# Performance work log

Hardware: AMD Instinct MI355X
Metric: run time of the kernel (lower is better)

Reference implementation:

```python
import jax, jax.numpy as jnp
import numpy as np

N, E, C, H, L, G, K, NC = 50000, 500000, 256, 128, 4, 64, 8, 2
EPS_MSG = 1e-7  # GENConv message eps
EPS_BN = 1e-5   # BatchNorm eps


def setup_inputs() -> dict:
    key = jax.random.key(0)
    ks = jax.random.split(key, 32)
    def nrm(k, shape, scale):
        return jax.random.normal(k, shape, dtype=jnp.float32) * scale
    sC = 1.0 / np.sqrt(C).astype(np.float32)
    sH = 1.0 / np.sqrt(H).astype(np.float32)
    s2H = 1.0 / np.sqrt(2 * H).astype(np.float32)
    return dict(
        x=nrm(ks[0], (N, C), 1.0),
        edge_index=jax.random.randint(ks[1], (2, E), 0, N, dtype=jnp.int32),
        edge_attr=jax.random.uniform(ks[2], (E, 1), dtype=jnp.float32),
        batch=jnp.sort(jax.random.randint(ks[3], (N,), 0, G, dtype=jnp.int32)),
        clinical=nrm(ks[4], (G, K), 1.0),
        lin_src_w=nrm(ks[5], (C, H), sC), lin_src_b=nrm(ks[6], (H,), 0.01),
        lin_dst_w=nrm(ks[7], (C, H), sC), lin_dst_b=nrm(ks[8], (H,), 0.01),
        edge_w=nrm(ks[9], (L, 1, H), 1.0), edge_b=nrm(ks[10], (L, H), 0.01),
        t=0.1 + 0.01 * jax.random.normal(ks[11], (L,), dtype=jnp.float32),
        mlp_w1=nrm(ks[12], (L, H, 2 * H), sH), mlp_b1=nrm(ks[13], (L, 2 * H), 0.01),
        mlp_bn_g=1.0 + nrm(ks[14], (L, 2 * H), 0.1), mlp_bn_b=nrm(ks[15], (L, 2 * H), 0.1),
        mlp_bn_m=nrm(ks[16], (L, 2 * H), 0.1),
        mlp_bn_v=1.0 + jax.random.uniform(ks[17], (L, 2 * H), dtype=jnp.float32),
        mlp_w2=nrm(ks[18], (L, 2 * H, H), s2H), mlp_b2=nrm(ks[19], (L, H), 0.01),
        norm_g=1.0 + nrm(ks[20], (L, H), 0.1), norm_b=nrm(ks[21], (L, H), 0.1),
        norm_m=nrm(ks[22], (L, H), 0.1),
        norm_v=1.0 + jax.random.uniform(ks[23], (L, H), dtype=jnp.float32),
        cls_w=nrm(ks[24], (H + K, NC), 1.0 / np.sqrt(H + K).astype(np.float32)),
        cls_b=nrm(ks[25], (NC,), 0.01),
    )


def _bn(h, g, b, m, v):
    # eval-mode BatchNorm with running stats
    return g * (h - m) * jax.lax.rsqrt(v + EPS_BN) + b


def reference(x, edge_index, edge_attr, batch, clinical,
              lin_src_w, lin_src_b, lin_dst_w, lin_dst_b,
              edge_w, edge_b, t,
              mlp_w1, mlp_b1, mlp_bn_g, mlp_bn_b, mlp_bn_m, mlp_bn_v,
              mlp_w2, mlp_b2, norm_g, norm_b, norm_m, norm_v,
              cls_w, cls_b):
    n = x.shape[0]
    g_count = clinical.shape[0]
    src, dst = edge_index[0], edge_index[1]
    n_layers = t.shape[0]

    def genconv(xs, xd, l):
        # xs: source features feeding messages [N,H]; xd: dst skip features [N,H]
        e = edge_attr @ edge_w[l] + edge_b[l]               # [E,H]
        msg = jax.nn.relu(xs[src] + e) + EPS_MSG            # [E,H]
        z = msg * t[l]
        zmax = jax.ops.segment_max(z, dst, num_segments=n)  # [N,H]
        zmax = jnp.where(jnp.isfinite(zmax), zmax, 0.0)
        ez = jnp.exp(z - zmax[dst])
        denom = jax.ops.segment_sum(ez, dst, num_segments=n)
        agg = jax.ops.segment_sum(msg * ez, dst, num_segments=n) / jnp.maximum(denom, 1e-16)
        out = agg + xd
        # internal MLP [H, 2H, H]: Linear -> BN -> ReLU -> Linear
        hmid = jax.nn.relu(_bn(out @ mlp_w1[l] + mlp_b1[l],
                               mlp_bn_g[l], mlp_bn_b[l], mlp_bn_m[l], mlp_bn_v[l]))
        return hmid @ mlp_w2[l] + mlp_b2[l]

    # layer 0: conv only (per DeepGCN.forward); lin_src / lin_dst project C -> H
    xs0 = x @ lin_src_w + lin_src_b
    xd0 = x @ lin_dst_w + lin_dst_b
    h = genconv(xs0, xd0, 0)

    # layers 1..L-1: res+ block (norm -> act -> conv, residual add); dropout = identity (eval)
    for l in range(1, n_layers):
        r = jax.nn.relu(_bn(h, norm_g[l], norm_b[l], norm_m[l], norm_v[l]))
        h = h + genconv(r, r, l)

    # final norm/act from layer 0
    h = jax.nn.relu(_bn(h, norm_g[0], norm_b[0], norm_m[0], norm_v[0]))

    # global mean pool over graphs
    cnt = jax.ops.segment_sum(jnp.ones((n,), h.dtype), batch, num_segments=g_count)
    pooled = jax.ops.segment_sum(h, batch, num_segments=g_count) / jnp.maximum(cnt, 1.0)[:, None]

    z = jnp.concatenate([pooled, clinical], axis=1)
    return z @ cls_w + cls_b  # [G, num_classes]; squeeze is a no-op for G>1, NC=2
```

## Files before the change

### kernel.cpp

```cpp
#include <hip/hip_runtime.h>
#include <math.h>

#define Nn 50000
#define MPAD 50048
#define Ee 500000
#define Cc 256
#define Hh 128
#define Ll 4
#define Gg 64
#define Kk 8
#define NCc 2

#define NB 196

typedef __attribute__((ext_vector_type(8))) short short8;
typedef __attribute__((ext_vector_type(4))) float f32x4;
typedef __attribute__((ext_vector_type(2))) float f32x2;

#define RFL __builtin_amdgcn_readfirstlane

__device__ __forceinline__ unsigned short f2bf(float f) {
    union { float f; unsigned int u; } v;
    v.f = f;
    unsigned int u = v.u;
    return (unsigned short)((u + 0x7FFFu + ((u >> 16) & 1u)) >> 16);
}
__device__ __forceinline__ float bf2f(unsigned short s) {
    union { float f; unsigned int u; } v;
    v.u = ((unsigned int)s) << 16;
    return v.f;
}
__device__ __forceinline__ float bf2f_lo(unsigned int u) {
    union { float f; unsigned int u; } v;
    v.u = u << 16;
    return v.f;
}
__device__ __forceinline__ float bf2f_hi(unsigned int u) {
    union { float f; unsigned int u; } v;
    v.u = u & 0xffff0000u;
    return v.f;
}


__global__ void hist_kernel(const int* __restrict__ dst, int* __restrict__ deg) {
    int e = blockIdx.x * 256 + threadIdx.x;
    if (e < Ee) atomicAdd(&deg[dst[e]], 1);
}

__global__ __launch_bounds__(256) void bsum_kernel(const int* __restrict__ deg,
                                                   int* __restrict__ bsum) {
    __shared__ int ws[4];
    int t = threadIdx.x;
    int i = blockIdx.x * 256 + t;
    int v = (i < Nn) ? deg[i] : 0;
#pragma unroll
    for (int o = 32; o; o >>= 1) v += __shfl_down(v, o, 64);
    if ((t & 63) == 0) ws[t >> 6] = v;
    __syncthreads();
    if (t == 0) bsum[blockIdx.x] = ws[0] + ws[1] + ws[2] + ws[3];
}

__global__ __launch_bounds__(256) void bscan_kernel(const int* __restrict__ bsum,
                                                    int* __restrict__ boff,
                                                    int* __restrict__ off) {
    __shared__ int sc[256];
    int t = threadIdx.x;
    int v = (t < NB) ? bsum[t] : 0;
    sc[t] = v;
    __syncthreads();
    for (int o = 1; o < 256; o <<= 1) {
        int u = (t >= o) ? sc[t - o] : 0;
        __syncthreads();
        sc[t] += u;
        __syncthreads();
    }
    if (t < NB) boff[t] = sc[t] - v;
    if (t == NB - 1) off[Nn] = sc[t];
}

__global__ __launch_bounds__(256) void offsets_kernel(const int* __restrict__ deg,
                                                      const int* __restrict__ boff,
                                                      int* __restrict__ off,
                                                      int* __restrict__ pos) {
    __shared__ int sc[256];
    int t = threadIdx.x;
    int i = blockIdx.x * 256 + t;
    int v = (i < Nn) ? deg[i] : 0;
    sc[t] = v;
    __syncthreads();
    for (int o = 1; o < 256; o <<= 1) {
        int u = (t >= o) ? sc[t - o] : 0;
        __syncthreads();
        sc[t] += u;
        __syncthreads();
    }
    int excl = sc[t] - v + boff[blockIdx.x];
    if (i < Nn) {
        off[i] = excl;
        pos[i] = excl;
    }
}

__global__ void scatter_kernel(const int* __restrict__ src, const int* __restrict__ dst,
                               const float* __restrict__ attr, int* __restrict__ pos,
                               int2* __restrict__ sedge) {
    int e = blockIdx.x * 256 + threadIdx.x;
    if (e < Ee) {
        int d = dst[e];
        int p = atomicAdd(&pos[d], 1);
        sedge[p] = make_int2(src[e], __float_as_int(attr[e]));
    }
}


__global__ void wconv_kernel(const float* __restrict__ lin_src_w,
                             const float* __restrict__ lin_dst_w,
                             const float* __restrict__ mlp_w1,
                             const float* __restrict__ mlp_w2,
                             unsigned short* __restrict__ wt) {
    int idx = blockIdx.x * 256 + threadIdx.x;
    if (idx >= 327680) return;
    float val;
    if (idx < 65536) {
        int n = idx >> 8, k = idx & 255;
        val = (n < 128) ? lin_src_w[k * 128 + n] : lin_dst_w[k * 128 + (n - 128)];
    } else if (idx < 196608) {
        int r = idx - 65536;
        int l = r >> 15, e = r & 32767;
        int n = e >> 7, k = e & 127;
        val = mlp_w1[(size_t)l * 32768 + k * 256 + n];
    } else {
        int r = idx - 196608;
        int l = r >> 15, e = r & 32767;
        int n = e >> 8, k = e & 255;
        val = mlp_w2[(size_t)l * 32768 + k * 128 + n];
    }
    wt[idx] = f2bf(val);
}


__global__ __launch_bounds__(256) void xconv_kernel(const float* __restrict__ x,
                                                    unsigned short* __restrict__ xbf) {
    int idx = blockIdx.x * 256 + threadIdx.x;
    if (idx >= (Nn * Cc) / 8) return;
    const float4* p = (const float4*)(x) + (size_t)idx * 2;
    float4 v0 = p[0], v1 = p[1];
    unsigned short t[8];
    t[0] = f2bf(v0.x); t[1] = f2bf(v0.y); t[2] = f2bf(v0.z); t[3] = f2bf(v0.w);
    t[4] = f2bf(v1.x); t[5] = f2bf(v1.y); t[6] = f2bf(v1.z); t[7] = f2bf(v1.w);
    *(short8*)(xbf + (size_t)idx * 8) = *(short8*)t;
}

#define GLOAD16(gp, lp)                                                                       \
    __builtin_amdgcn_global_load_lds(                                                         \
        (const __attribute__((address_space(1))) unsigned int*)(gp),                          \
        (__attribute__((address_space(3))) unsigned int*)(lp), 16, 0, 0)


__global__ __launch_bounds__(256) void proj_kernel(
    const unsigned short* __restrict__ A, const unsigned short* __restrict__ Bt,
    const float* __restrict__ bias, const float* __restrict__ bias2,
    unsigned short* __restrict__ Cout) {
    __shared__ __align__(16) unsigned short SH[24576];
    int tid = threadIdx.x;
    int wave = tid >> 6, lane = tid & 63;
    int wr = wave >> 1, wc = wave & 1;
    int lrow = lane & 15, quad = lane >> 4;
    int m0 = blockIdx.y * 128, n0 = blockIdx.x * 128;
    const int K = 256;

    const unsigned short* ag0 = A + (size_t)(m0 + (tid >> 2)) * K + (tid & 3) * 8;
    const unsigned short* ag1 = A + (size_t)(m0 + 64 + (tid >> 2)) * K + (tid & 3) * 8;
    const unsigned short* bg0 = Bt + (size_t)(n0 + (tid >> 2)) * K + (tid & 3) * 8;
    const unsigned short* bg1 = Bt + (size_t)(n0 + 64 + (tid >> 2)) * K + (tid & 3) * 8;

    f32x4 acc[4][4];
#pragma unroll
    for (int i = 0; i < 4; i++)
#pragma unroll
        for (int j = 0; j < 4; j++) acc[i][j] = (f32x4){0.f, 0.f, 0.f, 0.f};

    auto stage = [&](int buf, int koff) {
        GLOAD16(ag0 + koff, SH + buf * 4096 + wave * 512);
        GLOAD16(ag1 + koff, SH + buf * 4096 + 2048 + wave * 512);
        GLOAD16(bg0 + koff, SH + 12288 + buf * 4096 + wave * 512);
        GLOAD16(bg1 + koff, SH + 12288 + buf * 4096 + 2048 + wave * 512);
    };

    const int ntiles = 8;
    stage(0, 0);
    stage(1, 32);
    for (int t = 0; t < ntiles; ++t) {
        if (t + 1 < ntiles) {
            asm volatile("s_waitcnt vmcnt(4)\n\ts_barrier" ::: "memory");
        } else {
            asm volatile("s_waitcnt vmcnt(0)\n\ts_barrier" ::: "memory");
        }
        if (t + 2 < ntiles) stage((t + 2) % 3, (t + 2) * 32);
        int cur = t % 3;
        const unsigned short* As = SH + cur * 4096;
        const unsigned short* Bs = SH + 12288 + cur * 4096;
        short8 af[4], bfr[4];
#pragma unroll
        for (int mt = 0; mt < 4; mt++)
            af[mt] = *(const short8*)&As[(wr * 64 + mt * 16 + lrow) * 32 + quad * 8];
#pragma unroll
        for (int nf = 0; nf < 4; nf++)
            bfr[nf] = *(const short8*)&Bs[(wc * 64 + nf * 16 + lrow) * 32 + quad * 8];
#pragma unroll
        for (int mt = 0; mt < 4; mt++)
#pragma unroll
            for (int nf = 0; nf < 4; nf++)
                acc[mt][nf] = __builtin_amdgcn_mfma_f32_16x16x32_bf16(af[mt], bfr[nf],
                                                                     acc[mt][nf], 0, 0, 0);
    }

    __syncthreads();
    unsigned short* Cl = SH;
#pragma unroll
    for (int nf = 0; nf < 4; nf++) {
        int gc = n0 + wc * 64 + nf * 16 + lrow;
        float bs = (gc >= 128) ? bias2[gc - 128] : bias[gc];
        int col = wc * 64 + nf * 16 + lrow;
#pragma unroll
        for (int mt = 0; mt < 4; mt++)
#pragma unroll
            for (int r = 0; r < 4; r++)
                Cl[(wr * 64 + mt * 16 + quad * 4 + r) * 128 + col] = f2bf(acc[mt][nf][r] + bs);
    }
    __syncthreads();
#pragma unroll
    for (int p = 0; p < 8; p++) {
        int vid = p * 256 + tid;
        int row = vid >> 4, cg = (vid & 15) * 8;
        short8 v = *(const short8*)&Cl[row * 128 + cg];
        *(short8*)(Cout + (size_t)(m0 + row) * 256 + n0 + cg) = v;
    }
}


__global__ __launch_bounds__(256) void mlp_kernel(
    const unsigned short* __restrict__ A,
    const unsigned short* __restrict__ W1,
    const unsigned short* __restrict__ W2,
    const float* __restrict__ b1, const float* __restrict__ bn_g,
    const float* __restrict__ bn_b, const float* __restrict__ bn_m,
    const float* __restrict__ bn_v, const float* __restrict__ b2,
    const float* __restrict__ pn_g, const float* __restrict__ pn_b,
    const float* __restrict__ pn_m, const float* __restrict__ pn_v,
    float* __restrict__ hbuf, unsigned short* __restrict__ rbuf, int rmw) {
    __shared__ __align__(16) unsigned short LDS_[23040];
    unsigned short* Ap = LDS_;
    unsigned short* B1 = LDS_ + 8192;
    unsigned short* Hm = LDS_;
    unsigned short* B2 = LDS_ + 16896;

    int tid = threadIdx.x;
    int wave = tid >> 6, lane = tid & 63;
    int lrow = lane & 15, quad = lane >> 4;
    int m0 = blockIdx.x * 64;

    {
        const unsigned short* as = A + (size_t)(m0 + (tid >> 2)) * 128 + (tid & 3) * 8;
#pragma unroll
        for (int t = 0; t < 4; t++) GLOAD16(as + t * 32, Ap + t * 2048 + wave * 512);
    }
    const unsigned short* w1base = W1 + (size_t)(tid >> 2) * 128 + (tid & 3) * 8;
    auto stageB1 = [&](int s, int b) {
        int h = s >> 2, t = s & 3;
        const unsigned short* p = w1base + (size_t)h * 128 * 128 + t * 32;
        GLOAD16(p, B1 + b * 4096 + wave * 512);
        GLOAD16(p + (size_t)64 * 128, B1 + b * 4096 + 2048 + wave * 512);
    };
    stageB1(0, 0);
    stageB1(1, 1);

    f32x4 acc1a[4][2], acc1b[4][2];
#pragma unroll
    for (int i = 0; i < 4; i++)
#pragma unroll
        for (int j = 0; j < 2; j++) {
            acc1a[i][j] = (f32x4){0.f, 0.f, 0.f, 0.f};
            acc1b[i][j] = (f32x4){0.f, 0.f, 0.f, 0.f};
        }

#pragma unroll
    for (int t = 0; t < 4; t++) {
        asm volatile("s_waitcnt vmcnt(2)\n\ts_barrier" ::: "memory");
        stageB1(t + 2, (t + 2) % 3);
        const unsigned short* Apan = Ap + t * 2048;
        const unsigned short* Bs = B1 + (t % 3) * 4096;
        short8 af[4], bfr[2];
#pragma unroll
        for (int mt = 0; mt < 4; mt++)
            af[mt] = *(const short8*)&Apan[(mt * 16 + lrow) * 32 + quad * 8];
#pragma unroll
        for (int nf = 0; nf < 2; nf++)
            bfr[nf] = *(const short8*)&Bs[(wave * 32 + nf * 16 + lrow) * 32 + quad * 8];
#pragma unroll
        for (int mt = 0; mt < 4; mt++)
#pragma unroll
            for (int nf = 0; nf < 2; nf++)
                acc1a[mt][nf] = __builtin_amdgcn_mfma_f32_16x16x32_bf16(af[mt], bfr[nf],
                                                                       acc1a[mt][nf], 0, 0, 0);
    }
#pragma unroll
    for (int t = 0; t < 4; t++) {
        if (t < 3) {
            asm volatile("s_waitcnt vmcnt(2)\n\ts_barrier" ::: "memory");
        } else {
            asm volatile("s_waitcnt vmcnt(0)\n\ts_barrier" ::: "memory");
        }
        if (t < 2) stageB1(6 + t, (6 + t) % 3);
        const unsigned short* Apan = Ap + t * 2048;
        const unsigned short* Bs = B1 + ((4 + t) % 3) * 4096;
        short8 af[4], bfr[2];
#pragma unroll
        for (int mt = 0; mt < 4; mt++)
            af[mt] = *(const short8*)&Apan[(mt * 16 + lrow) * 32 + quad * 8];
#pragma unroll
        for (int nf = 0; nf < 2; nf++)
            bfr[nf] = *(const short8*)&Bs[(wave * 32 + nf * 16 + lrow) * 32 + quad * 8];
#pragma unroll
        for (int mt = 0; mt < 4; mt++)
#pragma unroll
            for (int nf = 0; nf < 2; nf++)
                acc1b[mt][nf] = __builtin_amdgcn_mfma_f32_16x16x32_bf16(af[mt], bfr[nf],
                                                                       acc1b[mt][nf], 0, 0, 0);
    }
    __syncthreads();

    const unsigned short* w2base = W2 + (size_t)(tid >> 2) * 256 + (tid & 3) * 8;
    auto stageB2 = [&](int s, int b) {
        int h = s >> 3, t = s & 7;
        GLOAD16(w2base + (size_t)h * 64 * 256 + t * 32, B2 + b * 2048 + wave * 512);
    };
    stageB2(0, 0);
    stageB2(1, 1);

#pragma unroll
    for (int nf = 0; nf < 2; nf++) {
        int gc = wave * 32 + nf * 16 + lrow;
        float bs = b1[gc];
        float g = bn_g[gc], bb = bn_b[gc], mm = bn_m[gc];
        float inv = rsqrtf(bn_v[gc] + 1e-5f);
#pragma unroll
        for (int mt = 0; mt < 4; mt++)
#pragma unroll
            for (int r = 0; r < 4; r++) {
                float v = acc1a[mt][nf][r] + bs;
                v = fmaxf(g * (v - mm) * inv + bb, 0.f);
                Hm[(mt * 16 + quad * 4 + r) * 264 + gc] = f2bf(v);
            }
    }
#pragma unroll
    for (int nf = 0; nf < 2; nf++) {
        int gc = 128 + wave * 32 + nf * 16 + lrow;
        float bs = b1[gc];
        float g = bn_g[gc], bb = bn_b[gc], mm = bn_m[gc];
        float inv = rsqrtf(bn_v[gc] + 1e-5f);
#pragma unroll
        for (int mt = 0; mt < 4; mt++)
#pragma unroll
            for (int r = 0; r < 4; r++) {
                float v = acc1b[mt][nf][r] + bs;
                v = fmaxf(g * (v - mm) * inv + bb, 0.f);
                Hm[(mt * 16 + quad * 4 + r) * 264 + gc] = f2bf(v);
            }
    }
    __syncthreads();

    f32x4 acc2a[4], acc2b[4];
#pragma unroll
    for (int i = 0; i < 4; i++) {
        acc2a[i] = (f32x4){0.f, 0.f, 0.f, 0.f};
        acc2b[i] = (f32x4){0.f, 0.f, 0.f, 0.f};
    }
#pragma unroll
    for (int t = 0; t < 8; t++) {
        asm volatile("s_waitcnt vmcnt(1)\n\ts_barrier" ::: "memory");
        stageB2(t + 2, (t + 2) % 3);
        const unsigned short* Bs = B2 + (t % 3) * 2048;
        short8 af[4];
#pragma unroll
        for (int mt = 0; mt < 4; mt++)
            af[mt] = *(const short8*)&Hm[(mt * 16 + lrow) * 264 + t * 32 + quad * 8];
        short8 bf = *(const short8*)&Bs[(wave * 16 + lrow) * 32 + quad * 8];
#pragma unroll
        for (int mt = 0; mt < 4; mt++)
            acc2a[mt] = __builtin_amdgcn_mfma_f32_16x16x32_bf16(af[mt], bf, acc2a[mt], 0, 0, 0);
    }
#pragma unroll
    for (int t = 0; t < 8; t++) {
        if (t < 7) {
            asm volatile("s_waitcnt vmcnt(1)\n\ts_barrier" ::: "memory");
        } else {
            asm volatile("s_waitcnt vmcnt(0)\n\ts_barrier" ::: "memory");
        }
        if (t < 6) stageB2(10 + t, (10 + t) % 3);
        const unsigned short* Bs = B2 + ((8 + t) % 3) * 2048;
        short8 af[4];
#pragma unroll
        for (int mt = 0; mt < 4; mt++)
            af[mt] = *(const short8*)&Hm[(mt * 16 + lrow) * 264 + t * 32 + quad * 8];
        short8 bf = *(const short8*)&Bs[(wave * 16 + lrow) * 32 + quad * 8];
#pragma unroll
        for (int mt = 0; mt < 4; mt++)
            acc2b[mt] = __builtin_amdgcn_mfma_f32_16x16x32_bf16(af[mt], bf, acc2b[mt], 0, 0, 0);
    }
    __syncthreads();

    float* C2 = (float*)LDS_;
    {
        int gc0 = wave * 16 + lrow, gc1 = 64 + wave * 16 + lrow;
        float bs0 = b2[gc0], bs1 = b2[gc1];
#pragma unroll
        for (int mt = 0; mt < 4; mt++)
#pragma unroll
            for (int r = 0; r < 4; r++) {
                C2[(mt * 16 + quad * 4 + r) * 132 + gc0] = acc2a[mt][r] + bs0;
                C2[(mt * 16 + quad * 4 + r) * 132 + gc1] = acc2b[mt][r] + bs1;
            }
    }
    __syncthreads();
#pragma unroll
    for (int p = 0; p < 8; p++) {
        int vid = p * 256 + tid;
        int row = vid >> 5, c4 = (vid & 31) * 4;
        f32x4 v = *(const f32x4*)&C2[row * 132 + c4];
        float* hp = hbuf + (size_t)(m0 + row) * 128 + c4;
        if (rmw) v += *(const f32x4*)hp;
        *(f32x4*)hp = v;
        if (pn_g) {
            f32x4 pg = *(const f32x4*)&pn_g[c4];
            f32x4 pb = *(const f32x4*)&pn_b[c4];
            f32x4 pm = *(const f32x4*)&pn_m[c4];
            f32x4 pv = *(const f32x4*)&pn_v[c4];
            float r0 = fmaxf(pg[0] * (v[0] - pm[0]) * rsqrtf(pv[0] + 1e-5f) + pb[0], 0.f);
            float r1 = fmaxf(pg[1] * (v[1] - pm[1]) * rsqrtf(pv[1] + 1e-5f) + pb[1], 0.f);
            float r2 = fmaxf(pg[2] * (v[2] - pm[2]) * rsqrtf(pv[2] + 1e-5f) + pb[2], 0.f);
            float r3 = fmaxf(pg[3] * (v[3] - pm[3]) * rsqrtf(pv[3] + 1e-5f) + pb[3], 0.f);
            unsigned int w0 = (unsigned int)f2bf(r0) | ((unsigned int)f2bf(r1) << 16);
            unsigned int w1 = (unsigned int)f2bf(r2) | ((unsigned int)f2bf(r3) << 16);
            uint2 pk = make_uint2(w0, w1);
            *(uint2*)(rbuf + (size_t)(m0 + row) * 128 + c4) = pk;
        }
    }
}


template <int XSS>
__global__ __launch_bounds__(256) void agg_kernel(
    const unsigned short* __restrict__ xs,
    const unsigned short* __restrict__ xd, int xds,
    const int2* __restrict__ sedge, const int* __restrict__ off,
    const float* __restrict__ ew, const float* __restrict__ eb,
    const float* __restrict__ tptr, unsigned short* __restrict__ outb) {
    int wave = threadIdx.x >> 6;
    int lane = threadIdx.x & 63;
    int d0 = blockIdx.x * 8 + wave * 2;
    int d1 = d0 + 1;
    int f0 = lane * 2;
    unsigned int uda = *(const unsigned int*)(xd + (size_t)d0 * xds + f0);
    unsigned int udb = *(const unsigned int*)(xd + (size_t)d1 * xds + f0);
    f32x2 wv = *(const f32x2*)(ew + f0);
    f32x2 bv = *(const f32x2*)(eb + f0);
    float c = tptr[0] * 1.44269504088896f;
    const f32x2 zz = {0.f, 0.f};
    int s0a = RFL(off[d0]), s1a = RFL(off[d0 + 1]);
    int s0b = RFL(off[d1]), s1b = RFL(off[d1 + 1]);
    f32x2 dena = {0.f, 0.f}, numa = {0.f, 0.f};
    f32x2 denb = {0.f, 0.f}, numb = {0.f, 0.f};

#define EDGE2(u, av, den, num)                                      \
    {                                                               \
        f32x2 xv = {bf2f_lo(u), bf2f_hi(u)};                        \
        f32x2 m = __builtin_elementwise_max(xv + bv + (av)*wv, zz); \
        f32x2 e;                                                    \
        e.x = __builtin_amdgcn_exp2f(m.x * c);                      \
        e.y = __builtin_amdgcn_exp2f(m.y * c);                      \
        den += e;                                                   \
        num += m * e;                                               \
    }
#define EDGE2M(u, av, mk, den, num)                                 \
    {                                                               \
        f32x2 xv = {bf2f_lo(u), bf2f_hi(u)};                        \
        f32x2 m = __builtin_elementwise_max(xv + bv + (av)*wv, zz); \
        f32x2 e;                                                    \
        e.x = __builtin_amdgcn_exp2f(m.x * c) * (mk);               \
        e.y = __builtin_amdgcn_exp2f(m.y * c) * (mk);               \
        den += e;                                                   \
        num += m * e;                                               \
    }
#define LOADMETA(jv, ii, aa)                                   \
    {                                                          \
        int4 q0 = *(const int4*)(sedge + (jv));                \
        int4 q1 = *(const int4*)(sedge + (jv) + 2);            \
        int4 q2 = *(const int4*)(sedge + (jv) + 4);            \
        int4 q3 = *(const int4*)(sedge + (jv) + 6);            \
        ii[0] = RFL(q0.x); aa[0] = __int_as_float(RFL(q0.y));  \
        ii[1] = RFL(q0.z); aa[1] = __int_as_float(RFL(q0.w));  \
        ii[2] = RFL(q1.x); aa[2] = __int_as_float(RFL(q1.y));  \
        ii[3] = RFL(q1.z); aa[3] = __int_as_float(RFL(q1.w));  \
        ii[4] = RFL(q2.x); aa[4] = __int_as_float(RFL(q2.y));  \
        ii[5] = RFL(q2.z); aa[5] = __int_as_float(RFL(q2.w));  \
        ii[6] = RFL(q3.x); aa[6] = __int_as_float(RFL(q3.y));  \
        ii[7] = RFL(q3.z); aa[7] = __int_as_float(RFL(q3.w));  \
    }
#define GATHER8(ii, uu)                                                          \
    _Pragma("unroll") for (int k = 0; k < 8; k++) uu[k] =                        \
        *(const unsigned int*)(xs + (size_t)ii[k] * XSS + f0);

    int ja = s0a, jb = s0b;
    while (ja + 8 <= s1a && jb + 8 <= s1b) {
        int ia[8], ib[8];
        float aa[8], ab[8];
        LOADMETA(ja, ia, aa)
        LOADMETA(jb, ib, ab)
        unsigned int ua[8], ub[8];
        GATHER8(ia, ua)
        GATHER8(ib, ub)
#pragma unroll
        for (int k = 0; k < 8; k++) EDGE2(ua[k], aa[k], dena, numa)
#pragma unroll
        for (int k = 0; k < 8; k++) EDGE2(ub[k], ab[k], denb, numb)
        ja += 8;
        jb += 8;
    }
    while (ja + 8 <= s1a) {
        int ia[8];
        float aa[8];
        LOADMETA(ja, ia, aa)
        unsigned int ua[8];
        GATHER8(ia, ua)
#pragma unroll
        for (int k = 0; k < 8; k++) EDGE2(ua[k], aa[k], dena, numa)
        ja += 8;
    }
    while (jb + 8 <= s1b) {
        int ib[8];
        float ab[8];
        LOADMETA(jb, ib, ab)
        unsigned int ub[8];
        GATHER8(ib, ub)
#pragma unroll
        for (int k = 0; k < 8; k++) EDGE2(ub[k], ab[k], denb, numb)
        jb += 8;
    }
    if (ja < s1a || jb < s1b) {
        int lasta = (s1a > s0a) ? s1a - 1 : 0;
        int lastb = (s1b > s0b) ? s1b - 1 : 0;
        int ia[8], ib[8];
        float aa[8], ab[8], ma[8], mb[8];
#pragma unroll
        for (int k = 0; k < 8; k++) {
            int jj = ja + k;
            int cl = (jj < s1a) ? jj : lasta;
            int2 p = sedge[cl];
            ia[k] = RFL(p.x);
            aa[k] = __int_as_float(RFL(p.y));
            ma[k] = (jj < s1a) ? 1.f : 0.f;
            jj = jb + k;
            cl = (jj < s1b) ? jj : lastb;
            int2 q = sedge[cl];
            ib[k] = RFL(q.x);
            ab[k] = __int_as_float(RFL(q.y));
            mb[k] = (jj < s1b) ? 1.f : 0.f;
        }
        unsigned int ua[8], ub[8];
        GATHER8(ia, ua)
        GATHER8(ib, ub)
#pragma unroll
        for (int k = 0; k < 8; k++) EDGE2M(ua[k], aa[k], ma[k], dena, numa)
#pragma unroll
        for (int k = 0; k < 8; k++) EDGE2M(ub[k], ab[k], mb[k], denb, numb)
    }
#undef EDGE2
#undef EDGE2M
#undef LOADMETA
#undef GATHER8
    float a0 = (s1a > s0a) ? (numa.x / dena.x + 1e-7f) : 0.f;
    float a1 = (s1a > s0a) ? (numa.y / dena.y + 1e-7f) : 0.f;
    float b0 = (s1b > s0b) ? (numb.x / denb.x + 1e-7f) : 0.f;
    float b1 = (s1b > s0b) ? (numb.y / denb.y + 1e-7f) : 0.f;
    unsigned int lo = f2bf(a0 + bf2f_lo(uda));
    unsigned int hi = f2bf(a1 + bf2f_hi(uda));
    *(unsigned int*)(outb + (size_t)d0 * Hh + f0) = lo | (hi << 16);
    lo = f2bf(b0 + bf2f_lo(udb));
    hi = f2bf(b1 + bf2f_hi(udb));
    *(unsigned int*)(outb + (size_t)d1 * Hh + f0) = lo | (hi << 16);
}


#define PCHUNK 100

__global__ __launch_bounds__(128) void pool_kernel(
    const float* __restrict__ h, const int* __restrict__ batch,
    const float* __restrict__ g, const float* __restrict__ b,
    const float* __restrict__ m, const float* __restrict__ v,
    float* __restrict__ pooled, float* __restrict__ cnt) {
    int hh = threadIdx.x;
    int i0 = blockIdx.x * PCHUNK;
    int i1 = min(i0 + PCHUNK, Nn);
    if (i0 >= Nn) return;
    float gg = g[hh], bb = b[hh], mm = m[hh], inv = rsqrtf(v[hh] + 1e-5f);
    int cur = batch[i0];
    float sum = 0.f, c = 0.f;
    for (int i = i0; i < i1; i++) {
        int gid = batch[i];
        float val = fmaxf(gg * (h[(size_t)i * Hh + hh] - mm) * inv + bb, 0.f);
        if (gid != cur) {
            atomicAdd(&pooled[(size_t)cur * Hh + hh], sum);
            if (hh == 0) atomicAdd(&cnt[cur], c);
            cur = gid;
            sum = 0.f;
            c = 0.f;
        }
        sum += val;
        c += 1.f;
    }
    atomicAdd(&pooled[(size_t)cur * Hh + hh], sum);
    if (hh == 0) atomicAdd(&cnt[cur], c);
}


__global__ __launch_bounds__(128) void cls_kernel(const float* __restrict__ pooled,
                                                  const float* __restrict__ cnt,
                                                  const float* __restrict__ clinical,
                                                  const float* __restrict__ w,
                                                  const float* __restrict__ bias,
                                                  float* __restrict__ out) {
    int t = threadIdx.x;
    int g = t >> 1, c = t & 1;
    float inv = 1.f / fmaxf(cnt[g], 1.f);
    float s = bias[c];
    for (int j = 0; j < Hh; j++) s += pooled[g * Hh + j] * inv * w[j * NCc + c];
    for (int k = 0; k < Kk; k++) s += clinical[g * Kk + k] * w[(Hh + k) * NCc + c];
    out[g * NCc + c] = s;
}


extern "C" void kernel_launch(void* const* d_in, const int* in_sizes, int n_in,
                              void* d_out, int out_size, void* d_ws, size_t ws_size,
                              hipStream_t stream) {
    const float* x = (const float*)d_in[0];
    const int* eidx = (const int*)d_in[1];
    const float* eattr = (const float*)d_in[2];
    const int* batch = (const int*)d_in[3];
    const float* clinical = (const float*)d_in[4];
    const float* lin_src_w = (const float*)d_in[5];
    const float* lin_src_b = (const float*)d_in[6];
    const float* lin_dst_w = (const float*)d_in[7];
    const float* lin_dst_b = (const float*)d_in[8];
    const float* edge_w = (const float*)d_in[9];
    const float* edge_b = (const float*)d_in[10];
    const float* tt = (const float*)d_in[11];
    const float* mlp_w1 = (const float*)d_in[12];
    const float* mlp_b1 = (const float*)d_in[13];
    const float* bn_g = (const float*)d_in[14];
    const float* bn_b = (const float*)d_in[15];
    const float* bn_m = (const float*)d_in[16];
    const float* bn_v = (const float*)d_in[17];
    const float* mlp_w2 = (const float*)d_in[18];
    const float* mlp_b2 = (const float*)d_in[19];
    const float* norm_g = (const float*)d_in[20];
    const float* norm_b = (const float*)d_in[21];
    const float* norm_m = (const float*)d_in[22];
    const float* norm_v = (const float*)d_in[23];
    const float* cls_w = (const float*)d_in[24];
    const float* cls_b = (const float*)d_in[25];
    float* out = (float*)d_out;

    const int* src = eidx;
    const int* dst = eidx + Ee;

    char* ws = (char*)d_ws;
    size_t off_b = 0;
    auto alloc = [&](size_t bytes) -> void* {
        void* p = ws + off_b;
        off_b += (bytes + 255) & ~(size_t)255;
        return p;
    };
    int* deg = (int*)alloc((Nn + 1) * 4);
    float* pooled = (float*)alloc((size_t)Gg * Hh * 4);
    float* cntb = (float*)alloc(Gg * 4);
    unsigned short* xsd = (unsigned short*)alloc((size_t)MPAD * 256 * 2);
    unsigned short* rbuf = (unsigned short*)alloc((size_t)MPAD * Hh * 2);
    unsigned short* aggout = (unsigned short*)alloc((size_t)MPAD * Hh * 2);
    unsigned short* xbf = (unsigned short*)alloc((size_t)MPAD * 256 * 2);
    float* hbuf = (float*)alloc((size_t)MPAD * Hh * 4);
    int* offp = (int*)alloc((Nn + 1) * 4);
    int* pos = (int*)alloc((size_t)Nn * 4);
    int* bsum = (int*)alloc(NB * 4);
    int* boff = (int*)alloc(NB * 4);
    int2* sedge = (int2*)alloc((size_t)Ee * 8);
    unsigned short* wt = (unsigned short*)alloc((size_t)327680 * 2);

    hipMemsetAsync(deg, 0, 200192 + 32768 + 256, stream);

    hist_kernel<<<(Ee + 255) / 256, 256, 0, stream>>>(dst, deg);
    bsum_kernel<<<NB, 256, 0, stream>>>(deg, bsum);
    bscan_kernel<<<1, 256, 0, stream>>>(bsum, boff, offp);
    offsets_kernel<<<NB, 256, 0, stream>>>(deg, boff, offp, pos);
    scatter_kernel<<<(Ee + 255) / 256, 256, 0, stream>>>(src, dst, eattr, pos, sedge);
    wconv_kernel<<<1280, 256, 0, stream>>>(lin_src_w, lin_dst_w, mlp_w1, mlp_w2, wt);
    xconv_kernel<<<(Nn * Cc / 8 + 255) / 256, 256, 0, stream>>>(x, xbf);

    const unsigned short* wt_proj = wt;
    const unsigned short* wt_w1 = wt + 65536;
    const unsigned short* wt_w2 = wt + 196608;

    dim3 gproj(2, MPAD / 128);
    proj_kernel<<<gproj, 256, 0, stream>>>(xbf, wt_proj, lin_src_b, lin_dst_b, xsd);

    for (int l = 0; l < Ll; l++) {
        if (l == 0) {
            agg_kernel<256><<<Nn / 8, 256, 0, stream>>>(xsd, xsd + 128, 256, sedge, offp,
                                                        edge_w + l * Hh, edge_b + l * Hh,
                                                        tt + l, aggout);
        } else {
            agg_kernel<128><<<Nn / 8, 256, 0, stream>>>(rbuf, rbuf, Hh, sedge, offp,
                                                        edge_w + l * Hh, edge_b + l * Hh,
                                                        tt + l, aggout);
        }
        const float* png = (l < Ll - 1) ? (norm_g + (l + 1) * Hh) : nullptr;
        const float* pnb = (l < Ll - 1) ? (norm_b + (l + 1) * Hh) : nullptr;
        const float* pnm = (l < Ll - 1) ? (norm_m + (l + 1) * Hh) : nullptr;
        const float* pnv = (l < Ll - 1) ? (norm_v + (l + 1) * Hh) : nullptr;
        mlp_kernel<<<MPAD / 64, 256, 0, stream>>>(
            aggout, wt_w1 + (size_t)l * 32768, wt_w2 + (size_t)l * 32768,
            mlp_b1 + l * 2 * Hh, bn_g + l * 2 * Hh, bn_b + l * 2 * Hh,
            bn_m + l * 2 * Hh, bn_v + l * 2 * Hh, mlp_b2 + l * Hh,
            png, pnb, pnm, pnv, hbuf, rbuf, (l == 0) ? 0 : 1);
    }

    pool_kernel<<<(Nn + PCHUNK - 1) / PCHUNK, 128, 0, stream>>>(hbuf, batch, norm_g, norm_b,
                                                                norm_m, norm_v, pooled, cntb);
    cls_kernel<<<1, 128, 0, stream>>>(pooled, cntb, clinical, cls_w, cls_b, out);
}
```

Baseline: 492.3 us.

## Split each wave across two edges per step with 4-feature lanes in aggregation

```diff
diff --git a/kernel.cpp b/kernel.cpp
--- a/kernel.cpp
+++ b/kernel.cpp
@@ -458,137 +458,93 @@
     const float* __restrict__ tptr, unsigned short* __restrict__ outb) {
     int wave = threadIdx.x >> 6;
     int lane = threadIdx.x & 63;
-    int d0 = blockIdx.x * 8 + wave * 2;
-    int d1 = d0 + 1;
-    int f0 = lane * 2;
-    unsigned int uda = *(const unsigned int*)(xd + (size_t)d0 * xds + f0);
-    unsigned int udb = *(const unsigned int*)(xd + (size_t)d1 * xds + f0);
-    f32x2 wv = *(const f32x2*)(ew + f0);
-    f32x2 bv = *(const f32x2*)(eb + f0);
+    int d = blockIdx.x * 4 + wave;
+    int hw = lane >> 5;
+    int li = lane & 31;
+    int f0 = li * 4;
+    uint2 ud = *(const uint2*)(xd + (size_t)d * xds + f0);
+    f32x4 wv = *(const f32x4*)(ew + f0);
+    f32x4 bv = *(const f32x4*)(eb + f0);
     float c = tptr[0] * 1.44269504088896f;
-    const f32x2 zz = {0.f, 0.f};
-    int s0a = RFL(off[d0]), s1a = RFL(off[d0 + 1]);
-    int s0b = RFL(off[d1]), s1b = RFL(off[d1 + 1]);
-    f32x2 dena = {0.f, 0.f}, numa = {0.f, 0.f};
-    f32x2 denb = {0.f, 0.f}, numb = {0.f, 0.f};
-
-#define EDGE2(u, av, den, num)                                      \
-    {                                                               \
-        f32x2 xv = {bf2f_lo(u), bf2f_hi(u)};                        \
-        f32x2 m = __builtin_elementwise_max(xv + bv + (av)*wv, zz); \
-        f32x2 e;                                                    \
-        e.x = __builtin_amdgcn_exp2f(m.x * c);                      \
-        e.y = __builtin_amdgcn_exp2f(m.y * c);                      \
-        den += e;                                                   \
-        num += m * e;                                               \
-    }
-#define EDGE2M(u, av, mk, den, num)                                 \
-    {                                                               \
-        f32x2 xv = {bf2f_lo(u), bf2f_hi(u)};                        \
-        f32x2 m = __builtin_elementwise_max(xv + bv + (av)*wv, zz); \
-        f32x2 e;                                                    \
-        e.x = __builtin_amdgcn_exp2f(m.x * c) * (mk);               \
-        e.y = __builtin_amdgcn_exp2f(m.y * c) * (mk);               \
-        den += e;                                                   \
-        num += m * e;                                               \
-    }
-#define LOADMETA(jv, ii, aa)                                   \
-    {                                                          \
-        int4 q0 = *(const int4*)(sedge + (jv));                \
-        int4 q1 = *(const int4*)(sedge + (jv) + 2);            \
-        int4 q2 = *(const int4*)(sedge + (jv) + 4);            \
-        int4 q3 = *(const int4*)(sedge + (jv) + 6);            \
-        ii[0] = RFL(q0.x); aa[0] = __int_as_float(RFL(q0.y));  \
-        ii[1] = RFL(q0.z); aa[1] = __int_as_float(RFL(q0.w));  \
-        ii[2] = RFL(q1.x); aa[2] = __int_as_float(RFL(q1.y));  \
-        ii[3] = RFL(q1.z); aa[3] = __int_as_float(RFL(q1.w));  \
-        ii[4] = RFL(q2.x); aa[4] = __int_as_float(RFL(q2.y));  \
-        ii[5] = RFL(q2.z); aa[5] = __int_as_float(RFL(q2.w));  \
-        ii[6] = RFL(q3.x); aa[6] = __int_as_float(RFL(q3.y));  \
-        ii[7] = RFL(q3.z); aa[7] = __int_as_float(RFL(q3.w));  \
-    }
-#define GATHER8(ii, uu)                                                          \
-    _Pragma("unroll") for (int k = 0; k < 8; k++) uu[k] =                        \
-        *(const unsigned int*)(xs + (size_t)ii[k] * XSS + f0);
-
-    int ja = s0a, jb = s0b;
-    while (ja + 8 <= s1a && jb + 8 <= s1b) {
-        int ia[8], ib[8];
-        float aa[8], ab[8];
-        LOADMETA(ja, ia, aa)
-        LOADMETA(jb, ib, ab)
-        unsigned int ua[8], ub[8];
-        GATHER8(ia, ua)
-        GATHER8(ib, ub)
-#pragma unroll
-        for (int k = 0; k < 8; k++) EDGE2(ua[k], aa[k], dena, numa)
-#pragma unroll
-        for (int k = 0; k < 8; k++) EDGE2(ub[k], ab[k], denb, numb)
-        ja += 8;
-        jb += 8;
-    }
-    while (ja + 8 <= s1a) {
-        int ia[8];
-        float aa[8];
-        LOADMETA(ja, ia, aa)
-        unsigned int ua[8];
-        GATHER8(ia, ua)
-#pragma unroll
-        for (int k = 0; k < 8; k++) EDGE2(ua[k], aa[k], dena, numa)
-        ja += 8;
-    }
-    while (jb + 8 <= s1b) {
-        int ib[8];
-        float ab[8];
-        LOADMETA(jb, ib, ab)
-        unsigned int ub[8];
-        GATHER8(ib, ub)
-#pragma unroll
-        for (int k = 0; k < 8; k++) EDGE2(ub[k], ab[k], denb, numb)
-        jb += 8;
-    }
-    if (ja < s1a || jb < s1b) {
-        int lasta = (s1a > s0a) ? s1a - 1 : 0;
-        int lastb = (s1b > s0b) ? s1b - 1 : 0;
-        int ia[8], ib[8];
-        float aa[8], ab[8], ma[8], mb[8];
+    const f32x4 zz = {0.f, 0.f, 0.f, 0.f};
+    int s0 = RFL(off[d]), s1 = RFL(off[d + 1]);
+    f32x4 den = zz, num = zz;
+
+#define EDGE4(u, av)                                                            \
+    {                                                                           \
+        f32x4 xv = {bf2f_lo((u).x), bf2f_hi((u).x),                             \
+                    bf2f_lo((u).y), bf2f_hi((u).y)};                            \
+        f32x4 m = __builtin_elementwise_max(xv + bv + (av)*wv, zz);             \
+        f32x4 e;                                                                \
+        e.x = __builtin_amdgcn_exp2f(m.x * c);                                  \
+        e.y = __builtin_amdgcn_exp2f(m.y * c);                                  \
+        e.z = __builtin_amdgcn_exp2f(m.z * c);                                  \
+        e.w = __builtin_amdgcn_exp2f(m.w * c);                                  \
+        den += e;                                                               \
+        num += m * e;                                                           \
+    }
+#define EDGE4M(u, av, mk)                                                       \
+    {                                                                           \
+        f32x4 xv = {bf2f_lo((u).x), bf2f_hi((u).x),                             \
+                    bf2f_lo((u).y), bf2f_hi((u).y)};                            \
+        f32x4 m = __builtin_elementwise_max(xv + bv + (av)*wv, zz);             \
+        f32x4 e;                                                                \
+        e.x = __builtin_amdgcn_exp2f(m.x * c) * (mk);                           \
+        e.y = __builtin_amdgcn_exp2f(m.y * c) * (mk);                           \
+        e.z = __builtin_amdgcn_exp2f(m.z * c) * (mk);                           \
+        e.w = __builtin_amdgcn_exp2f(m.w * c) * (mk);                           \
+        den += e;                                                               \
+        num += m * e;                                                           \
+    }
+
+    int j = s0;
+    for (; j + 16 <= s1; j += 16) {
+        int2 mp[8];
+#pragma unroll
+        for (int k = 0; k < 8; k++) mp[k] = sedge[j + 2 * k + hw];
+        uint2 uu[8];
+#pragma unroll
+        for (int k = 0; k < 8; k++)
+            uu[k] = *(const uint2*)(xs + (size_t)mp[k].x * XSS + f0);
+#pragma unroll
+        for (int k = 0; k < 8; k++) EDGE4(uu[k], __int_as_float(mp[k].y))
+    }
+    if (j < s1) {
+        int last = s1 - 1;
+        int2 mp[8];
+        float mk[8];
 #pragma unroll
         for (int k = 0; k < 8; k++) {
-            int jj = ja + k;
-            int cl = (jj < s1a) ? jj : lasta;
-            int2 p = sedge[cl];
-            ia[k] = RFL(p.x);
-            aa[k] = __int_as_float(RFL(p.y));
-            ma[k] = (jj < s1a) ? 1.f : 0.f;
-            jj = jb + k;
-            cl = (jj < s1b) ? jj : lastb;
-            int2 q = sedge[cl];
-            ib[k] = RFL(q.x);
-            ab[k] = __int_as_float(RFL(q.y));
-            mb[k] = (jj < s1b) ? 1.f : 0.f;
-        }
-        unsigned int ua[8], ub[8];
-        GATHER8(ia, ua)
-        GATHER8(ib, ub)
-#pragma unroll
-        for (int k = 0; k < 8; k++) EDGE2M(ua[k], aa[k], ma[k], dena, numa)
-#pragma unroll
-        for (int k = 0; k < 8; k++) EDGE2M(ub[k], ab[k], mb[k], denb, numb)
-    }
-#undef EDGE2
-#undef EDGE2M
-#undef LOADMETA
-#undef GATHER8
-    float a0 = (s1a > s0a) ? (numa.x / dena.x + 1e-7f) : 0.f;
-    float a1 = (s1a > s0a) ? (numa.y / dena.y + 1e-7f) : 0.f;
-    float b0 = (s1b > s0b) ? (numb.x / denb.x + 1e-7f) : 0.f;
-    float b1 = (s1b > s0b) ? (numb.y / denb.y + 1e-7f) : 0.f;
-    unsigned int lo = f2bf(a0 + bf2f_lo(uda));
-    unsigned int hi = f2bf(a1 + bf2f_hi(uda));
-    *(unsigned int*)(outb + (size_t)d0 * Hh + f0) = lo | (hi << 16);
-    lo = f2bf(b0 + bf2f_lo(udb));
-    hi = f2bf(b1 + bf2f_hi(udb));
-    *(unsigned int*)(outb + (size_t)d1 * Hh + f0) = lo | (hi << 16);
+            int jj = j + 2 * k + hw;
+            int cl = (jj < s1) ? jj : last;
+            mp[k] = sedge[cl];
+            mk[k] = (jj < s1) ? 1.f : 0.f;
+        }
+        uint2 uu[8];
+#pragma unroll
+        for (int k = 0; k < 8; k++)
+            uu[k] = *(const uint2*)(xs + (size_t)mp[k].x * XSS + f0);
+#pragma unroll
+        for (int k = 0; k < 8; k++) EDGE4M(uu[k], __int_as_float(mp[k].y), mk[k])
+    }
+#undef EDGE4
+#undef EDGE4M
+#pragma unroll
+    for (int t = 0; t < 4; t++) {
+        den[t] += __shfl_xor(den[t], 32, 64);
+        num[t] += __shfl_xor(num[t], 32, 64);
+    }
+    if (hw == 0) {
+        float a0 = (s1 > s0) ? (num[0] / den[0] + 1e-7f) : 0.f;
+        float a1 = (s1 > s0) ? (num[1] / den[1] + 1e-7f) : 0.f;
+        float a2 = (s1 > s0) ? (num[2] / den[2] + 1e-7f) : 0.f;
+        float a3 = (s1 > s0) ? (num[3] / den[3] + 1e-7f) : 0.f;
+        unsigned int r0 = (unsigned int)f2bf(a0 + bf2f_lo(ud.x)) |
+                          ((unsigned int)f2bf(a1 + bf2f_hi(ud.x)) << 16);
+        unsigned int r1 = (unsigned int)f2bf(a2 + bf2f_lo(ud.y)) |
+                          ((unsigned int)f2bf(a3 + bf2f_hi(ud.y)) << 16);
+        *(uint2*)(outb + (size_t)d * Hh + f0) = make_uint2(r0, r1);
+    }
 }
 
 
@@ -715,11 +671,11 @@
 
     for (int l = 0; l < Ll; l++) {
         if (l == 0) {
-            agg_kernel<256><<<Nn / 8, 256, 0, stream>>>(xsd, xsd + 128, 256, sedge, offp,
+            agg_kernel<256><<<Nn / 4, 256, 0, stream>>>(xsd, xsd + 128, 256, sedge, offp,
                                                         edge_w + l * Hh, edge_b + l * Hh,
                                                         tt + l, aggout);
         } else {
-            agg_kernel<128><<<Nn / 8, 256, 0, stream>>>(rbuf, rbuf, Hh, sedge, offp,
+            agg_kernel<128><<<Nn / 4, 256, 0, stream>>>(rbuf, rbuf, Hh, sedge, offp,
                                                         edge_w + l * Hh, edge_b + l * Hh,
                                                         tt + l, aggout);
         }
```

Result: slower. 533.5 us (+8.4%).
